# Optimization experiments

Hardware: AMD Instinct MI355X
Metric: run time of the kernel (lower is better)

The kernel has to match this reference:

```python
import jax, jax.numpy as jnp
import numpy as np

N, E, G = 50000, 800000, 64   # nodes, edges, graphs in batch
H, C = 4, 64                  # GAT heads, per-head channels (concat=False -> averaged)
F_IN, D_OUT = 16, 32
NEG_SLOPE = 0.2


def setup_inputs():
    key = jax.random.key(0)
    ks = jax.random.split(key, 20)
    s = 0.05
    inp = {
        "x": jax.random.normal(ks[0], (N, F_IN), jnp.float32),
        "edge_index": jax.random.randint(ks[1], (2, E), 0, N, dtype=jnp.int32),
        "batch": jnp.sort(jax.random.randint(ks[2], (N,), 0, G, dtype=jnp.int32)),
        "Wp": jax.random.normal(ks[3], (F_IN, H * C // H), jnp.float32) * s,  # 16 -> 64
        "bp": jnp.zeros((64,), jnp.float32),
        "Wo": jax.random.normal(ks[4], (64, D_OUT), jnp.float32) * s,
        "bo": jnp.zeros((D_OUT,), jnp.float32),
    }
    for l in range(3):
        inp[f"W{l}"] = jax.random.normal(ks[5 + 3 * l], (64, H * C), jnp.float32) * s
        inp[f"as{l}"] = jax.random.normal(ks[6 + 3 * l], (H, C), jnp.float32) * s
        inp[f"ad{l}"] = jax.random.normal(ks[7 + 3 * l], (H, C), jnp.float32) * s
        inp[f"b{l}"] = jnp.zeros((C,), jnp.float32)
    return inp


def _gat_layer(h, src, dst, W, a_src, a_dst, b):
    # h: [N, 64] -> per-head features [N, H, C]
    hw = (h @ W).reshape(N, H, C)
    # per-node attention logits [N, H]
    al_s = jnp.sum(hw * a_src, axis=-1)
    al_d = jnp.sum(hw * a_dst, axis=-1)
    # per-edge logits (src contributes alpha_src, dst contributes alpha_dst)
    e = jax.nn.leaky_relu(al_s[src] + al_d[dst], NEG_SLOPE)  # [Et, H]
    # neighbor-wise softmax over edges grouped by destination node
    emax = jax.ops.segment_max(e, dst, num_segments=N)
    ex = jnp.exp(e - emax[dst])
    denom = jax.ops.segment_sum(ex, dst, num_segments=N)
    alpha = ex / denom[dst]                                   # [Et, H]
    # weighted scatter-add of source features to destinations
    msg = alpha[:, :, None] * hw[src]                         # [Et, H, C]
    out = jax.ops.segment_sum(msg, dst, num_segments=N)       # [N, H, C]
    return out.mean(axis=1) + b                               # concat=False: head mean


def reference(x, edge_index, batch, Wp, bp, W0, as0, ad0, b0,
              W1, as1, ad1, b1, W2, as2, ad2, b2, Wo, bo):
    # add self-loops once (PyG GATConv default add_self_loops=True)
    loop = jnp.arange(N, dtype=edge_index.dtype)
    src = jnp.concatenate([edge_index[0], loop])
    dst = jnp.concatenate([edge_index[1], loop])

    h = jax.nn.relu(x @ Wp + bp)
    for (W, a_s, a_d, b) in ((W0, as0, ad0, b0), (W1, as1, ad1, b1), (W2, as2, ad2, b2)):
        h = jax.nn.relu(_gat_layer(h, src, dst, W, a_s, a_d, b))

    # global mean pool over graphs
    sums = jax.ops.segment_sum(h, batch, num_segments=G)
    cnt = jax.ops.segment_sum(jnp.ones((N,), h.dtype), batch, num_segments=G)
    pooled = sums / jnp.maximum(cnt, 1.0)[:, None]
    return pooled @ Wo + bo
```

## Files before the change

kernel.cpp:

```cpp
#include <hip/hip_runtime.h>

#define NEG_SLOPE 0.2f

typedef __attribute__((ext_vector_type(8))) short bf16x8;
typedef __attribute__((ext_vector_type(4))) float f32x4;

__device__ __forceinline__ float lrelu(float x) { return x > 0.f ? x : NEG_SLOPE * x; }

__device__ __forceinline__ float bf2f(unsigned short u) {
  return __uint_as_float(((unsigned int)u) << 16);
}
__device__ __forceinline__ unsigned short f2bf(float f) {
  unsigned int u = __float_as_uint(f);
  u += 0x7fffu + ((u >> 16) & 1u);
  return (unsigned short)(u >> 16);
}

__global__ void proj_kernel(const float* __restrict__ x, const float* __restrict__ Wp,
                            const float* __restrict__ bp, unsigned short* __restrict__ h,
                            int n_nodes) {
  int idx = blockIdx.x * blockDim.x + threadIdx.x;
  int n = idx >> 6, c = idx & 63;
  if (n >= n_nodes) return;
  float acc = bp[c];
#pragma unroll
  for (int k = 0; k < 16; ++k) acc += x[n * 16 + k] * Wp[k * 64 + c];
  h[n * 64 + c] = f2bf(fmaxf(acc, 0.f));
}

__global__ void hist_kernel(const int* __restrict__ dst, int* __restrict__ deg, int e) {
  int i = blockIdx.x * blockDim.x + threadIdx.x;
  if (i < e) atomicAdd(&deg[dst[i]], 1);
}

__global__ __launch_bounds__(256) void scan_a(const int* __restrict__ deg, int* __restrict__ rowp,
                                              int* __restrict__ bsum, int n) {
  __shared__ int s[256];
  int t = threadIdx.x;
  int base = blockIdx.x * 1024 + t * 4;
  int d0 = (base + 0 < n) ? deg[base + 0] + 1 : 0;
  int d1 = (base + 1 < n) ? deg[base + 1] + 1 : 0;
  int d2 = (base + 2 < n) ? deg[base + 2] + 1 : 0;
  int d3 = (base + 3 < n) ? deg[base + 3] + 1 : 0;
  s[t] = d0 + d1 + d2 + d3;
  __syncthreads();
  for (int off = 1; off < 256; off <<= 1) {
    int v = 0;
    if (t >= off) v = s[t - off];
    __syncthreads();
    if (t >= off) s[t] += v;
    __syncthreads();
  }
  int p = (t == 0) ? 0 : s[t - 1];
  if (base + 0 < n) rowp[base + 0] = p;
  p += d0;
  if (base + 1 < n) rowp[base + 1] = p;
  p += d1;
  if (base + 2 < n) rowp[base + 2] = p;
  p += d2;
  if (base + 3 < n) rowp[base + 3] = p;
  if (t == 255) bsum[blockIdx.x] = s[255];
}

__global__ void scan_b(const int* __restrict__ bsum, int* __restrict__ bpre, int nb) {
  int t = threadIdx.x;
  int v = (t < nb) ? bsum[t] : 0;
  int orig = v;
#pragma unroll
  for (int off = 1; off < 64; off <<= 1) {
    int u = __shfl_up(v, off);
    if (t >= off) v += u;
  }
  bpre[t] = v - orig;
  if (t == 63) bpre[64] = v;
}

__global__ void scan_c(int* __restrict__ rowp, const int* __restrict__ bpre,
                       int* __restrict__ cnt, int* __restrict__ col, int n) {
  int i = blockIdx.x * blockDim.x + threadIdx.x;
  if (i < n) {
    int r = rowp[i] + bpre[i >> 10];
    rowp[i] = r;
    cnt[i] = 1;
    col[r] = i;
  }
  if (i == 0) rowp[n] = bpre[64];
}

__global__ void scatter_kernel(const int* __restrict__ src, const int* __restrict__ dst,
                               const int* __restrict__ rowp, int* __restrict__ cnt,
                               int* __restrict__ col, int e) {
  int i = blockIdx.x * blockDim.x + threadIdx.x;
  if (i < e) {
    int d = dst[i];
    int pos = rowp[d] + atomicAdd(&cnt[d], 1);
    col[pos] = src[i];
  }
}

__global__ void prep_wa3(const float* __restrict__ W0, const float* __restrict__ as0, const float* __restrict__ ad0,
                         const float* __restrict__ W1, const float* __restrict__ as1, const float* __restrict__ ad1,
                         const float* __restrict__ W2, const float* __restrict__ as2, const float* __restrict__ ad2,
                         float* __restrict__ Wa) {
  int l = blockIdx.x;
  const float* W  = l == 0 ? W0  : l == 1 ? W1  : W2;
  const float* as = l == 0 ? as0 : l == 1 ? as1 : as2;
  const float* ad = l == 0 ? ad0 : l == 1 ? ad1 : ad2;
  int t = threadIdx.x;
  int k = t >> 2, h = t & 3;
  float ss = 0.f, sd = 0.f;
  for (int c = 0; c < 64; ++c) {
    float w = W[k * 256 + h * 64 + c];
    ss += w * as[h * 64 + c];
    sd += w * ad[h * 64 + c];
  }
  Wa[l * 512 + k * 8 + h] = ss;
  Wa[l * 512 + k * 8 + 4 + h] = sd;
}

__global__ void prep_wsw(const float* __restrict__ W0, const float* __restrict__ W1,
                         const float* __restrict__ W2, const float* __restrict__ Wa,
                         unsigned short* __restrict__ Wsw, unsigned short* __restrict__ Wasw) {
  int l = blockIdx.x;
  const float* W = l == 0 ? W0 : l == 1 ? W1 : W2;
  int t = threadIdx.x;
  for (int s = t; s < 2048; s += 256) {
    int nt = s >> 7, kk = (s >> 6) & 1, lane = s & 63;
    int kq = lane >> 4, r = lane & 15;
#pragma unroll
    for (int j = 0; j < 8; ++j) {
      int k = kk * 32 + kq * 8 + j;
      Wsw[(size_t)l * 16384 + (size_t)s * 8 + j] = f2bf(W[k * 256 + nt * 16 + r]);
    }
  }
  if (t < 128) {
    int lane = t & 63, kq = lane >> 4, r = lane & 15;
    int kk = t >> 6;
#pragma unroll
    for (int j = 0; j < 8; ++j) {
      int k = kk * 32 + kq * 8 + j;
      float v = (r < 8) ? Wa[l * 512 + k * 8 + r] : 0.f;
      Wasw[l * 1024 + t * 8 + j] = f2bf(v);
    }
  }
}

__global__ __launch_bounds__(256) void hw_kernel(const unsigned short* __restrict__ hb,
                                                 const unsigned short* __restrict__ Wsw,
                                                 const unsigned short* __restrict__ Wasw,
                                                 unsigned short* __restrict__ hwb,
                                                 float* __restrict__ al_s, float* __restrict__ al_d,
                                                 int n_nodes) {
  int t = threadIdx.x;
  int w = t >> 6, lane = t & 63;
  int kq = lane >> 4, r16 = lane & 15;
  int n0 = blockIdx.x << 6;

  bf16x8 a[4][2];
#pragma unroll
  for (int m = 0; m < 4; ++m) {
    int row = min(n0 + m * 16 + r16, n_nodes - 1);
    const unsigned short* p = hb + (size_t)row * 64 + kq * 8;
    a[m][0] = *(const bf16x8*)(p);
    a[m][1] = *(const bf16x8*)(p + 32);
  }
  bf16x8 b[4][2];
#pragma unroll
  for (int nt = 0; nt < 4; ++nt) {
    int ntg = w * 4 + nt;
    const unsigned short* p = Wsw + ((size_t)ntg * 128 + lane) * 8;
    b[nt][0] = *(const bf16x8*)(p);
    b[nt][1] = *(const bf16x8*)(p + 512);
  }

  f32x4 acc[4][4];
#pragma unroll
  for (int m = 0; m < 4; ++m)
#pragma unroll
    for (int nt = 0; nt < 4; ++nt) acc[m][nt] = (f32x4){0.f, 0.f, 0.f, 0.f};

#pragma unroll
  for (int m = 0; m < 4; ++m)
#pragma unroll
    for (int nt = 0; nt < 4; ++nt) {
      acc[m][nt] = __builtin_amdgcn_mfma_f32_16x16x32_bf16(a[m][0], b[nt][0], acc[m][nt], 0, 0, 0);
      acc[m][nt] = __builtin_amdgcn_mfma_f32_16x16x32_bf16(a[m][1], b[nt][1], acc[m][nt], 0, 0, 0);
    }

#pragma unroll
  for (int m = 0; m < 4; ++m) {
#pragma unroll
    for (int j = 0; j < 4; ++j) {
      int row = n0 + m * 16 + kq * 4 + j;
      if (row < n_nodes) {
#pragma unroll
        for (int nt = 0; nt < 4; ++nt) {
          int col = (w * 4 + nt) * 16 + r16;
          hwb[(size_t)row * 256 + col] = f2bf(acc[m][nt][j]);
        }
      }
    }
  }

  bf16x8 ba0 = *(const bf16x8*)(Wasw + lane * 8);
  bf16x8 ba1 = *(const bf16x8*)(Wasw + (64 + lane) * 8);
  f32x4 accl = (f32x4){0.f, 0.f, 0.f, 0.f};
  accl = __builtin_amdgcn_mfma_f32_16x16x32_bf16(a[w][0], ba0, accl, 0, 0, 0);
  accl = __builtin_amdgcn_mfma_f32_16x16x32_bf16(a[w][1], ba1, accl, 0, 0, 0);
  if (r16 < 8) {
#pragma unroll
    for (int j = 0; j < 4; ++j) {
      int row = n0 + w * 16 + kq * 4 + j;
      if (row < n_nodes) {
        if (r16 < 4) al_s[row * 4 + r16] = accl[j];
        else         al_d[row * 4 + (r16 - 4)] = accl[j];
      }
    }
  }
}

__global__ __launch_bounds__(256) void gat_agg(const int* __restrict__ rowp, const int* __restrict__ col,
                                               const float* __restrict__ alS, const float* __restrict__ alD,
                                               const unsigned short* __restrict__ hwb,
                                               const float* __restrict__ bias,
                                               unsigned short* __restrict__ hout,
                                               int n_nodes) {
  int lane = threadIdx.x & 63;
  int node = blockIdx.x * 4 + (threadIdx.x >> 6);
  if (node >= n_nodes) return;
  int base = __builtin_amdgcn_readfirstlane(rowp[node]);
  int deg  = __builtin_amdgcn_readfirstlane(rowp[node + 1]) - base;
  int head = lane >> 4;
  float ald = alD[node * 4 + head];

  float a0 = 0.f, a1 = 0.f, a2 = 0.f, a3 = 0.f, denom = 0.f;
#pragma unroll 4
  for (int i = 0; i < deg; ++i) {
    int s = __builtin_amdgcn_readfirstlane(col[base + i]);
    float w = __expf(lrelu(alS[s * 4 + head] + ald));
    denom += w;
    ushort4 v = *(const ushort4*)(hwb + ((size_t)s << 8) + (lane << 2));
    a0 += w * bf2f(v.x);
    a1 += w * bf2f(v.y);
    a2 += w * bf2f(v.z);
    a3 += w * bf2f(v.w);
  }
  float inv = 1.f / denom;
  a0 *= inv; a1 *= inv; a2 *= inv; a3 *= inv;

  a0 += __shfl_xor(a0, 16); a0 += __shfl_xor(a0, 32);
  a1 += __shfl_xor(a1, 16); a1 += __shfl_xor(a1, 32);
  a2 += __shfl_xor(a2, 16); a2 += __shfl_xor(a2, 32);
  a3 += __shfl_xor(a3, 16); a3 += __shfl_xor(a3, 32);

  if (lane < 16) {
    float4 b = *(const float4*)(bias + lane * 4);
    ushort4 o;
    o.x = f2bf(fmaxf(0.25f * a0 + b.x, 0.f));
    o.y = f2bf(fmaxf(0.25f * a1 + b.y, 0.f));
    o.z = f2bf(fmaxf(0.25f * a2 + b.z, 0.f));
    o.w = f2bf(fmaxf(0.25f * a3 + b.w, 0.f));
    *(ushort4*)(hout + (size_t)node * 64 + lane * 4) = o;
  }
}

__global__ void pool_kernel(const unsigned short* __restrict__ h, const int* __restrict__ batch,
                            float* __restrict__ pool, float* __restrict__ pcnt, int n_nodes) {
  int c = threadIdx.x;
  int n0 = blockIdx.x * 64;
  int n1 = min(n0 + 64, n_nodes);
  float acc = 0.f;
  int run = 0;
  int gcur = batch[n0];
  for (int n = n0; n < n1; ++n) {
    int g = batch[n];
    if (g != gcur) {
      atomicAdd(&pool[gcur * 64 + c], acc);
      if (c == 0) atomicAdd(&pcnt[gcur], (float)run);
      acc = 0.f; run = 0; gcur = g;
    }
    acc += bf2f(h[(size_t)n * 64 + c]);
    ++run;
  }
  atomicAdd(&pool[gcur * 64 + c], acc);
  if (c == 0) atomicAdd(&pcnt[gcur], (float)run);
}

__global__ void out_kernel(const float* __restrict__ pool, const float* __restrict__ pcnt,
                           const float* __restrict__ Wo, const float* __restrict__ bo,
                           float* __restrict__ out, int g_total) {
  int idx = blockIdx.x * blockDim.x + threadIdx.x;
  if (idx >= g_total * 32) return;
  int g = idx >> 5, d = idx & 31;
  float inv = 1.f / fmaxf(pcnt[g], 1.f);
  float acc = bo[d];
#pragma unroll
  for (int c = 0; c < 64; ++c) acc += (pool[g * 64 + c] * inv) * Wo[c * 32 + d];
  out[idx] = acc;
}

extern "C" void kernel_launch(void* const* d_in, const int* in_sizes, int n_in,
                              void* d_out, int out_size, void* d_ws, size_t ws_size,
                              hipStream_t stream) {
  const float* x     = (const float*)d_in[0];
  const int*   ei    = (const int*)d_in[1];
  const int*   batch = (const int*)d_in[2];
  const float* Wp    = (const float*)d_in[3];
  const float* bp    = (const float*)d_in[4];
  const float* Wo    = (const float*)d_in[5];
  const float* bo    = (const float*)d_in[6];
  const float* Wl[3]  = {(const float*)d_in[7],  (const float*)d_in[11], (const float*)d_in[15]};
  const float* Asl[3] = {(const float*)d_in[8],  (const float*)d_in[12], (const float*)d_in[16]};
  const float* Adl[3] = {(const float*)d_in[9],  (const float*)d_in[13], (const float*)d_in[17]};
  const float* Bl[3]  = {(const float*)d_in[10], (const float*)d_in[14], (const float*)d_in[18]};

  const int N = in_sizes[0] / 16;
  const int E = in_sizes[1] / 2;
  const int G = out_size / 32;
  const int Et = E + N;
  const int* src = ei;
  const int* dst = ei + E;
  const int NB = (N + 1023) / 1024;

  char* ws = (char*)d_ws;
  size_t off = 0;
  auto take = [&](size_t bytes) -> void* {
    void* p = ws + off;
    off = (off + bytes + 255) & ~(size_t)255;
    return p;
  };
  unsigned short* h_a = (unsigned short*)take((size_t)N * 64 * 2);
  unsigned short* h_b = (unsigned short*)take((size_t)N * 64 * 2);
  unsigned short* hwb = (unsigned short*)take((size_t)N * 256 * 2);
  float* alS   = (float*)take((size_t)N * 4 * 4);
  float* alD   = (float*)take((size_t)N * 4 * 4);
  int*   deg   = (int*)take((size_t)N * 4);
  int*   cnt   = (int*)take((size_t)N * 4);
  int*   rowp  = (int*)take((size_t)(N + 1) * 4);
  int*   col   = (int*)take((size_t)Et * 4);
  int*   bsum  = (int*)take((size_t)64 * 4);
  int*   bpre  = (int*)take((size_t)65 * 4);
  float* Wa    = (float*)take((size_t)3 * 512 * 4);
  unsigned short* Wsw  = (unsigned short*)take((size_t)3 * 16384 * 2);
  unsigned short* Wasw = (unsigned short*)take((size_t)3 * 1024 * 2);
  float* pool  = (float*)take((size_t)G * 64 * 4);
  float* pcnt  = (float*)take((size_t)G * 4);
  (void)ws_size; (void)n_in;

  prep_wa3<<<3, 256, 0, stream>>>(Wl[0], Asl[0], Adl[0], Wl[1], Asl[1], Adl[1],
                                  Wl[2], Asl[2], Adl[2], Wa);
  prep_wsw<<<3, 256, 0, stream>>>(Wl[0], Wl[1], Wl[2], Wa, Wsw, Wasw);

  hipMemsetAsync(deg, 0, (size_t)N * 4, stream);
  hist_kernel<<<(E + 255) / 256, 256, 0, stream>>>(dst, deg, E);
  scan_a<<<NB, 256, 0, stream>>>(deg, rowp, bsum, N);
  scan_b<<<1, 64, 0, stream>>>(bsum, bpre, NB);
  scan_c<<<(N + 255) / 256, 256, 0, stream>>>(rowp, bpre, cnt, col, N);
  scatter_kernel<<<(E + 255) / 256, 256, 0, stream>>>(src, dst, rowp, cnt, col, E);

  proj_kernel<<<((size_t)N * 64 + 255) / 256, 256, 0, stream>>>(x, Wp, bp, h_a, N);

  const unsigned short* hin = h_a;
  unsigned short* hout = h_b;
  for (int l = 0; l < 3; ++l) {
    hw_kernel<<<(N + 63) / 64, 256, 0, stream>>>(hin, Wsw + (size_t)l * 16384,
                                                 Wasw + (size_t)l * 1024, hwb, alS, alD, N);
    gat_agg<<<(N + 3) / 4, 256, 0, stream>>>(rowp, col, alS, alD, hwb, Bl[l], hout, N);
    const unsigned short* tmp = hout;
    hout = (unsigned short*)hin;
    hin = tmp;
  }

  hipMemsetAsync(pool, 0, (size_t)G * 64 * 4, stream);
  hipMemsetAsync(pcnt, 0, (size_t)G * 4, stream);
  pool_kernel<<<(N + 63) / 64, 64, 0, stream>>>(hin, batch, pool, pcnt, N);
  out_kernel<<<(G * 32 + 255) / 256, 256, 0, stream>>>(pool, pcnt, Wo, bo, (float*)d_out, G);
}
```

Baseline: 443.6 us.

## Precompute edge attention weights lane-parallel into LDS before gather loop

The GAT aggregation kernel now loads up to 64 neighbor indices per chunk in parallel across lanes. It computes all four heads' exp(leaky_relu) weights at once and stages byte offset plus weight pairs in shared memory. The inner gather loop then reads the precomputed pair from LDS instead of doing a serial col load, an alS load and an exp per edge. Leaky ReLU becomes a branchless fmax. The cost is LDS usage and a chunked two-phase loop, and there is no explicit barrier, so correctness relies on per-wavefront lockstep ordering.

```diff
diff --git a/kernel.cpp b/kernel.cpp
--- a/kernel.cpp
+++ b/kernel.cpp
@@ -5,7 +5,7 @@
 typedef __attribute__((ext_vector_type(8))) short bf16x8;
 typedef __attribute__((ext_vector_type(4))) float f32x4;
 
-__device__ __forceinline__ float lrelu(float x) { return x > 0.f ? x : NEG_SLOPE * x; }
+__device__ __forceinline__ float lrelu(float x) { return fmaxf(x, NEG_SLOPE * x); }
 
 __device__ __forceinline__ float bf2f(unsigned short u) {
   return __uint_as_float(((unsigned int)u) << 16);
@@ -225,26 +225,47 @@
                                                const float* __restrict__ bias,
                                                unsigned short* __restrict__ hout,
                                                int n_nodes) {
-  int lane = threadIdx.x & 63;
-  int node = blockIdx.x * 4 + (threadIdx.x >> 6);
+  __shared__ uint2 pw[4][64 * 4];
+  int t = threadIdx.x;
+  int wslot = t >> 6, lane = t & 63;
+  int node = blockIdx.x * 4 + wslot;
   if (node >= n_nodes) return;
-  int base = __builtin_amdgcn_readfirstlane(rowp[node]);
-  int deg  = __builtin_amdgcn_readfirstlane(rowp[node + 1]) - base;
+  int base = rowp[node];
+  int degv = rowp[node + 1] - base;
   int head = lane >> 4;
-  float ald = alD[node * 4 + head];
+  unsigned int laneoff = (unsigned int)lane << 3;
+  float4 ald4 = *(const float4*)(alD + (size_t)node * 4);
 
   float a0 = 0.f, a1 = 0.f, a2 = 0.f, a3 = 0.f, denom = 0.f;
+
+  for (int c0 = 0; c0 < degv; c0 += 64) {
+    int cnt = min(64, degv - c0);
+    if (lane < cnt) {
+      int s = col[base + c0 + lane];
+      float4 as4 = *(const float4*)(alS + (size_t)s * 4);
+      unsigned int ab = (unsigned int)s << 9;
+      float w0 = __expf(lrelu(as4.x + ald4.x));
+      float w1 = __expf(lrelu(as4.y + ald4.y));
+      float w2 = __expf(lrelu(as4.z + ald4.z));
+      float w3 = __expf(lrelu(as4.w + ald4.w));
+      pw[wslot][lane * 4 + 0] = make_uint2(ab, __float_as_uint(w0));
+      pw[wslot][lane * 4 + 1] = make_uint2(ab, __float_as_uint(w1));
+      pw[wslot][lane * 4 + 2] = make_uint2(ab, __float_as_uint(w2));
+      pw[wslot][lane * 4 + 3] = make_uint2(ab, __float_as_uint(w3));
+    }
 #pragma unroll 4
-  for (int i = 0; i < deg; ++i) {
-    int s = __builtin_amdgcn_readfirstlane(col[base + i]);
-    float w = __expf(lrelu(alS[s * 4 + head] + ald));
-    denom += w;
-    ushort4 v = *(const ushort4*)(hwb + ((size_t)s << 8) + (lane << 2));
-    a0 += w * bf2f(v.x);
-    a1 += w * bf2f(v.y);
-    a2 += w * bf2f(v.z);
-    a3 += w * bf2f(v.w);
-  }
+    for (int i = 0; i < cnt; ++i) {
+      uint2 p = pw[wslot][i * 4 + head];
+      float w = __uint_as_float(p.y);
+      uint2 v = *(const uint2*)((const char*)hwb + (p.x + laneoff));
+      denom += w;
+      a0 += w * __uint_as_float(v.x << 16);
+      a1 += w * __uint_as_float(v.x & 0xffff0000u);
+      a2 += w * __uint_as_float(v.y << 16);
+      a3 += w * __uint_as_float(v.y & 0xffff0000u);
+    }
+  }
+
   float inv = 1.f / denom;
   a0 *= inv; a1 *= inv; a2 *= inv; a3 *= inv;
 
```

Measured after the change: 413.3 us. 6.8% less time.
